# Optimization experiments

Hardware: AMD Instinct MI355X
Metric: run time of the kernel (lower is better)

The kernel has to match this reference:

```python
import jax, jax.numpy as jnp
import numpy as np

EMBED = 2048
NUM_HEADS = 32
HEAD_DIM = EMBED // NUM_HEADS  # 64 (original head dim; sets the scaling)
RANK_KQ = 1024
RANK_V = 1024
DK = RANK_KQ // NUM_HEADS  # 32 low-rank kq head dim
DV = RANK_V // NUM_HEADS   # 32 low-rank v head dim
B, S = 2, 2048


def setup_inputs() -> dict:
    key = jax.random.key(0)
    ks = jax.random.split(key, 10)
    std = 0.02
    hidden_states = jax.random.normal(ks[0], (B, S, EMBED), dtype=jnp.float32)
    # causal additive mask, shape (B, 1, S, S) as asserted in forward
    neg = jnp.finfo(jnp.float32).min
    causal = jnp.where(jnp.tril(jnp.ones((S, S), dtype=bool)), 0.0, neg)
    attention_mask = jnp.broadcast_to(causal[None, None], (B, 1, S, S)).astype(jnp.float32)
    Wq = jax.random.normal(ks[1], (RANK_KQ, EMBED), dtype=jnp.float32) * std
    bq = jax.random.normal(ks[2], (RANK_KQ,), dtype=jnp.float32) * std
    Wk = jax.random.normal(ks[3], (RANK_KQ, EMBED), dtype=jnp.float32) * std
    bk = jax.random.normal(ks[4], (RANK_KQ,), dtype=jnp.float32) * std
    Wv = jax.random.normal(ks[5], (RANK_V, EMBED), dtype=jnp.float32) * std
    bv = jax.random.normal(ks[6], (RANK_V,), dtype=jnp.float32) * std
    Wo = jax.random.normal(ks[7], (EMBED, RANK_V), dtype=jnp.float32) * std
    bo = jax.random.normal(ks[8], (EMBED,), dtype=jnp.float32) * std
    return {"hidden_states": hidden_states, "attention_mask": attention_mask,
            "Wq": Wq, "bq": bq, "Wk": Wk, "bk": bk, "Wv": Wv, "bv": bv,
            "Wo": Wo, "bo": bo}


def reference(hidden_states, attention_mask, Wq, bq, Wk, bk, Wv, bv, Wo, bo):
    bsz, tgt_len, _ = hidden_states.shape
    scaling = HEAD_DIM ** (-0.5)  # uses ORIGINAL head_dim, not low-rank dim

    def split_heads(x, d):  # (b, s, H*d) -> (b, H, s, d)
        return x.reshape(bsz, -1, NUM_HEADS, d).transpose(0, 2, 1, 3)

    q = split_heads((hidden_states @ Wq.T + bq) * scaling, DK)
    k = split_heads(hidden_states @ Wk.T + bk, DK)
    v = split_heads(hidden_states @ Wv.T + bv, DV)

    # scores: (b, H, tgt, src)
    attn = jnp.einsum('bhqd,bhkd->bhqk', q, k)
    attn = attn + attention_mask  # broadcast over heads
    attn = jnp.maximum(attn, jnp.finfo(attn.dtype).min)
    attn = jax.nn.softmax(attn, axis=-1)

    out = jnp.einsum('bhqk,bhkd->bhqd', attn, v)  # (b, H, tgt, DV)
    out = out.transpose(0, 2, 1, 3).reshape(bsz, tgt_len, RANK_V)
    return out @ Wo.T + bo
```

## Files before the change

kernel.cpp:

```cpp
#include <hip/hip_runtime.h>
#include <stdint.h>

typedef __attribute__((ext_vector_type(8))) short bf16x8;
typedef __attribute__((ext_vector_type(4))) float f32x4;
typedef unsigned short ushort_t;

#define AS1 __attribute__((address_space(1)))
#define AS3 __attribute__((address_space(3)))

static __device__ __forceinline__ ushort_t f2b(float f) {
    union { float f; unsigned u; } x; x.f = f;
    unsigned r = x.u + 0x7fffu + ((x.u >> 16) & 1u);
    return (ushort_t)(r >> 16);
}
static __device__ __forceinline__ f32x4 mfma16(bf16x8 a, bf16x8 b, f32x4 c) {
    return __builtin_amdgcn_mfma_f32_16x16x32_bf16(a, b, c, 0, 0, 0);
}
static __device__ __forceinline__ void gl_lds16(const ushort_t* g, ushort_t* l) {
    __builtin_amdgcn_global_load_lds((const AS1 void*)g, (AS3 void*)l, 16, 0, 0);
}

__global__ __launch_bounds__(256)
void cvt_bf16(const float* __restrict__ s, ushort_t* __restrict__ d, int n8)
{
    int i = blockIdx.x * 256 + threadIdx.x;
    if (i >= n8) return;
    const float* p = s + (size_t)i * 8;
    f32x4 a = *(const f32x4*)p;
    f32x4 b = *(const f32x4*)(p + 4);
    bf16x8 r;
#pragma unroll
    for (int j = 0; j < 4; ++j) { r[j] = (short)f2b(a[j]); r[j+4] = (short)f2b(b[j]); }
    *(bf16x8*)(d + (size_t)i * 8) = r;
}

__global__ __launch_bounds__(256)
void cvt_w3(const float* __restrict__ wq, const float* __restrict__ wk,
            const float* __restrict__ wv, ushort_t* __restrict__ d)
{
    const float* s = (blockIdx.y == 0) ? wq : (blockIdx.y == 1) ? wk : wv;
    ushort_t* dst = d + (size_t)blockIdx.y * 2097152;
    int i = blockIdx.x * 256 + threadIdx.x;
    const float* p = s + (size_t)i * 8;
    f32x4 a = *(const f32x4*)p;
    f32x4 b = *(const f32x4*)(p + 4);
    bf16x8 r;
#pragma unroll
    for (int j = 0; j < 4; ++j) { r[j] = (short)f2b(a[j]); r[j+4] = (short)f2b(b[j]); }
    *(bf16x8*)(dst + (size_t)i * 8) = r;
}

__global__ __launch_bounds__(256, 2)
void gemm_nt(const ushort_t* __restrict__ A, const ushort_t* __restrict__ B,
             const float* __restrict__ b0, const float* __restrict__ b1,
             const float* __restrict__ b2, void* __restrict__ Cv,
             int M, int N, int K, float scale, int epi)
{
    __shared__ __align__(16) ushort_t As[128 * 32];
    __shared__ __align__(16) ushort_t Bs[128 * 32];
    const int tid = threadIdx.x;
    const int wave = tid >> 6, lane = tid & 63;
    const int l16 = lane & 15, quad = lane >> 4;
    const int bm = blockIdx.x * 128, bn = blockIdx.y * 128;
    const int wm = (wave >> 1) * 64, wn = (wave & 1) * 64;

    f32x4 acc[4][4];
#pragma unroll
    for (int i = 0; i < 4; ++i)
#pragma unroll
        for (int j = 0; j < 4; ++j) acc[i][j] = (f32x4){0.f, 0.f, 0.f, 0.f};

    for (int k0 = 0; k0 < K; k0 += 32) {
        __syncthreads();
#pragma unroll
        for (int i = 0; i < 2; ++i) {
            int chunk = i * 256 + tid;
            int row = chunk >> 2, c8 = chunk & 3;
            gl_lds16(A + (size_t)(bm + row) * K + k0 + c8 * 8, As + chunk * 8);
            gl_lds16(B + (size_t)(bn + row) * K + k0 + c8 * 8, Bs + chunk * 8);
        }
        __syncthreads();
        bf16x8 af[4], bfr[4];
#pragma unroll
        for (int i = 0; i < 4; ++i)
            af[i] = *(const bf16x8*)(As + (wm + i * 16 + l16) * 32 + quad * 8);
#pragma unroll
        for (int j = 0; j < 4; ++j)
            bfr[j] = *(const bf16x8*)(Bs + (wn + j * 16 + l16) * 32 + quad * 8);
#pragma unroll
        for (int i = 0; i < 4; ++i)
#pragma unroll
            for (int j = 0; j < 4; ++j)
                acc[i][j] = mfma16(af[i], bfr[j], acc[i][j]);
    }

#pragma unroll
    for (int i = 0; i < 4; ++i) {
#pragma unroll
        for (int j = 0; j < 4; ++j) {
            int col = bn + wn + j * 16 + l16;
            if (epi == 0) {
                float bvs = b0[col];
#pragma unroll
                for (int r = 0; r < 4; ++r) {
                    int row = bm + wm + i * 16 + quad * 4 + r;
                    ((float*)Cv)[(size_t)row * N + col] = (acc[i][j][r] + bvs) * scale;
                }
            } else {
                int mat = col >> 10, nc = col & 1023;
                float sc = (mat == 0) ? 0.125f : 1.0f;
                const float* bp = (mat == 0) ? b0 : (mat == 1) ? b1 : b2;
                float bvs = bp[nc];
                int h = nc >> 5, d = nc & 31;
                ushort_t* dst = (ushort_t*)Cv + (size_t)mat * 4194304;
#pragma unroll
                for (int r = 0; r < 4; ++r) {
                    int row = bm + wm + i * 16 + quad * 4 + r;
                    int b = row >> 11, s = row & 2047;
                    float v = (acc[i][j][r] + bvs) * sc;
                    dst[(((size_t)(b * 32 + h) * 2048 + s) << 5) + d] = f2b(v);
                }
            }
        }
    }
}

__global__ __launch_bounds__(256, 4)
void attn(const ushort_t* __restrict__ Q, const ushort_t* __restrict__ Kg,
          const ushort_t* __restrict__ V, ushort_t* __restrict__ Ctx)
{
    __shared__ __align__(16) ushort_t Ks[64 * 40];
    __shared__ __align__(16) ushort_t Vt[32 * 72];
    __shared__ __align__(16) ushort_t Ps[4][32 * 72];
    const int tid = threadIdx.x, wave = tid >> 6, lane = tid & 63;
    const int l16 = lane & 15, quad = lane >> 4;
    const int bh = blockIdx.x;
    const int qt = blockIdx.y;
    const ushort_t* Qh = Q + (size_t)bh * 2048 * 32;
    const ushort_t* Kh = Kg + (size_t)bh * 2048 * 32;
    const ushort_t* Vh = V + (size_t)bh * 2048 * 32;
    const int q0 = qt * 128 + wave * 32;

    bf16x8 qf0 = *(const bf16x8*)(Qh + (size_t)(q0 + l16) * 32 + quad * 8);
    bf16x8 qf1 = *(const bf16x8*)(Qh + (size_t)(q0 + 16 + l16) * 32 + quad * 8);

    f32x4 o00 = (f32x4){0.f,0.f,0.f,0.f}, o01 = o00, o10 = o00, o11 = o00;
    float rs0[4] = {0.f,0.f,0.f,0.f}, rs1[4] = {0.f,0.f,0.f,0.f};

    const int row = tid >> 2, c8 = tid & 3;
    const int nch = 2 * qt + 2;
    for (int c = 0; c < nch; ++c) {
        const int kv0 = c * 64;
        bf16x8 kv8 = *(const bf16x8*)(Kh + (size_t)(kv0 + row) * 32 + c8 * 8);
        bf16x8 vv  = *(const bf16x8*)(Vh + (size_t)(kv0 + row) * 32 + c8 * 8);
        __syncthreads();
        *(bf16x8*)(Ks + row * 40 + c8 * 8) = kv8;
#pragma unroll
        for (int j = 0; j < 8; ++j)
            Vt[(c8 * 8 + j) * 72 + row] = (ushort_t)vv[j];
        __syncthreads();

        if (kv0 <= q0 + 31) {
            f32x4 st0[4], st1[4];
#pragma unroll
            for (int t = 0; t < 4; ++t) {
                bf16x8 kf = *(const bf16x8*)(Ks + (t * 16 + l16) * 40 + quad * 8);
                st0[t] = mfma16(qf0, kf, (f32x4){0.f,0.f,0.f,0.f});
                st1[t] = mfma16(qf1, kf, (f32x4){0.f,0.f,0.f,0.f});
            }
#pragma unroll
            for (int t = 0; t < 4; ++t) {
                const int kk = kv0 + t * 16 + l16;
#pragma unroll
                for (int r = 0; r < 4; ++r) {
                    const int qr = q0 + quad * 4 + r;
                    float p0 = (kk <= qr) ? __expf(st0[t][r]) : 0.f;
                    rs0[r] += p0;
                    Ps[wave][(quad * 4 + r) * 72 + t * 16 + l16] = f2b(p0);
                    float p1 = (kk <= qr + 16) ? __expf(st1[t][r]) : 0.f;
                    rs1[r] += p1;
                    Ps[wave][(16 + quad * 4 + r) * 72 + t * 16 + l16] = f2b(p1);
                }
            }
            asm volatile("s_waitcnt lgkmcnt(0)" ::: "memory");
#pragma unroll
            for (int ks = 0; ks < 2; ++ks) {
                bf16x8 v0 = *(const bf16x8*)(Vt + (l16) * 72 + ks * 32 + quad * 8);
                bf16x8 v1 = *(const bf16x8*)(Vt + (16 + l16) * 72 + ks * 32 + quad * 8);
                bf16x8 p0 = *(const bf16x8*)(&Ps[wave][l16 * 72 + ks * 32 + quad * 8]);
                bf16x8 p1 = *(const bf16x8*)(&Ps[wave][(16 + l16) * 72 + ks * 32 + quad * 8]);
                o00 = mfma16(p0, v0, o00);
                o01 = mfma16(p0, v1, o01);
                o10 = mfma16(p1, v0, o10);
                o11 = mfma16(p1, v1, o11);
            }
        }
    }

#pragma unroll
    for (int r = 0; r < 4; ++r) {
#pragma unroll
        for (int off = 1; off < 16; off <<= 1) {
            rs0[r] += __shfl_xor(rs0[r], off);
            rs1[r] += __shfl_xor(rs1[r], off);
        }
    }

    const int b = bh >> 5, h = bh & 31;
#pragma unroll
    for (int r = 0; r < 4; ++r) {
        const int qr = q0 + quad * 4 + r;
        float inv0 = 1.0f / rs0[r];
        float inv1 = 1.0f / rs1[r];
        size_t base0 = ((size_t)b * 2048 + qr) * 1024 + h * 32;
        size_t base1 = ((size_t)b * 2048 + qr + 16) * 1024 + h * 32;
        Ctx[base0 + l16]      = f2b(o00[r] * inv0);
        Ctx[base0 + 16 + l16] = f2b(o01[r] * inv0);
        Ctx[base1 + l16]      = f2b(o10[r] * inv1);
        Ctx[base1 + 16 + l16] = f2b(o11[r] * inv1);
    }
}

extern "C" void kernel_launch(void* const* d_in, const int* in_sizes, int n_in,
                              void* d_out, int out_size, void* d_ws, size_t ws_size,
                              hipStream_t stream)
{
    const float* H  = (const float*)d_in[0];
    const float* Wq = (const float*)d_in[2];
    const float* bq = (const float*)d_in[3];
    const float* Wk = (const float*)d_in[4];
    const float* bk = (const float*)d_in[5];
    const float* Wv = (const float*)d_in[6];
    const float* bv = (const float*)d_in[7];
    const float* Wo = (const float*)d_in[8];
    const float* bo = (const float*)d_in[9];

    ushort_t* Hb   = (ushort_t*)d_ws;
    ushort_t* Wcat = Hb   + (size_t)8388608;
    ushort_t* Qb   = Wcat + (size_t)6291456;
    ushort_t* Kb   = Qb   + (size_t)4194304;
    ushort_t* Vb   = Kb   + (size_t)4194304;
    ushort_t* Ctx  = Vb   + (size_t)4194304;
    ushort_t* Wob  = Hb;

    dim3 blk(256, 1, 1);
    hipLaunchKernelGGL(cvt_bf16, dim3(4096, 1, 1), blk, 0, stream, H, Hb, 1048576);
    hipLaunchKernelGGL(cvt_w3, dim3(1024, 3, 1), blk, 0, stream, Wq, Wk, Wv, Wcat);

    hipLaunchKernelGGL(gemm_nt, dim3(32, 24, 1), blk, 0, stream,
                       Hb, Wcat, bq, bk, bv, (void*)Qb, 4096, 3072, 2048, 1.0f, 2);

    hipLaunchKernelGGL(cvt_bf16, dim3(1024, 1, 1), blk, 0, stream, Wo, Wob, 262144);

    hipLaunchKernelGGL(attn, dim3(64, 16, 1), blk, 0, stream, Qb, Kb, Vb, Ctx);

    hipLaunchKernelGGL(gemm_nt, dim3(32, 16, 1), blk, 0, stream,
                       Ctx, Wob, bo, bo, bo, d_out, 4096, 2048, 1024, 1.0f, 0);
}
```

Baseline: 299.8 us.

## Store V transposed from QKV GEMM and drop LDS staging in attention

The QKV projection epilogue now writes V in a transposed per-head layout (d-major, seq contiguous) using packed 8-byte stores. The attention kernel then loads K and V fragments straight from global memory into registers, which removes the shared-memory K/V staging, the scalar transpose into LDS, and both block-wide barriers per chunk. It also computes S^T so each lane holds one query column, packs P with v_cvt_pk_bf16_f32 into vectorized LDS writes, skips the mask on fully unmasked chunks, and loops each wave only over its own causal range. The cost is redundant global K/V reads per wave, since the four waves no longer share a staged tile, which depends on cache hits.

```diff
diff --git a/kernel.cpp b/kernel.cpp
--- a/kernel.cpp
+++ b/kernel.cpp
@@ -18,6 +18,11 @@
 }
 static __device__ __forceinline__ void gl_lds16(const ushort_t* g, ushort_t* l) {
     __builtin_amdgcn_global_load_lds((const AS1 void*)g, (AS3 void*)l, 16, 0, 0);
+}
+static __device__ __forceinline__ unsigned pk2(float a, float b) {
+    unsigned r;
+    asm("v_cvt_pk_bf16_f32 %0, %1, %2" : "=v"(r) : "v"(a), "v"(b));
+    return r;
 }
 
 __global__ __launch_bounds__(256)
@@ -108,17 +113,28 @@
                 }
             } else {
                 int mat = col >> 10, nc = col & 1023;
-                float sc = (mat == 0) ? 0.125f : 1.0f;
                 const float* bp = (mat == 0) ? b0 : (mat == 1) ? b1 : b2;
                 float bvs = bp[nc];
                 int h = nc >> 5, d = nc & 31;
-                ushort_t* dst = (ushort_t*)Cv + (size_t)mat * 4194304;
-#pragma unroll
-                for (int r = 0; r < 4; ++r) {
-                    int row = bm + wm + i * 16 + quad * 4 + r;
-                    int b = row >> 11, s = row & 2047;
-                    float v = (acc[i][j][r] + bvs) * sc;
-                    dst[(((size_t)(b * 32 + h) * 2048 + s) << 5) + d] = f2b(v);
+                if (mat == 2) {
+                    int row0 = bm + wm + i * 16 + quad * 4;
+                    int b = row0 >> 11, s = row0 & 2047;
+                    ushort_t* dst = (ushort_t*)Cv + (size_t)2 * 4194304
+                                  + ((size_t)(b * 32 + h) * 32 + d) * 2048 + s;
+                    uint2 w;
+                    w.x = ((unsigned)f2b(acc[i][j][1] + bvs) << 16) | f2b(acc[i][j][0] + bvs);
+                    w.y = ((unsigned)f2b(acc[i][j][3] + bvs) << 16) | f2b(acc[i][j][2] + bvs);
+                    *(uint2*)dst = w;
+                } else {
+                    float sc = (mat == 0) ? 0.125f : 1.0f;
+                    ushort_t* dst = (ushort_t*)Cv + (size_t)mat * 4194304;
+#pragma unroll
+                    for (int r = 0; r < 4; ++r) {
+                        int row = bm + wm + i * 16 + quad * 4 + r;
+                        int b = row >> 11, s = row & 2047;
+                        float v = (acc[i][j][r] + bvs) * sc;
+                        dst[(((size_t)(b * 32 + h) * 2048 + s) << 5) + d] = f2b(v);
+                    }
                 }
             }
         }
@@ -127,91 +143,89 @@
 
 __global__ __launch_bounds__(256, 4)
 void attn(const ushort_t* __restrict__ Q, const ushort_t* __restrict__ Kg,
-          const ushort_t* __restrict__ V, ushort_t* __restrict__ Ctx)
-{
-    __shared__ __align__(16) ushort_t Ks[64 * 40];
-    __shared__ __align__(16) ushort_t Vt[32 * 72];
+          const ushort_t* __restrict__ VT, ushort_t* __restrict__ Ctx)
+{
     __shared__ __align__(16) ushort_t Ps[4][32 * 72];
     const int tid = threadIdx.x, wave = tid >> 6, lane = tid & 63;
-    const int l16 = lane & 15, quad = lane >> 4;
+    const int l16 = lane & 15, quad = lane >> 4, quad4 = quad * 4;
     const int bh = blockIdx.x;
     const int qt = blockIdx.y;
-    const ushort_t* Qh = Q + (size_t)bh * 2048 * 32;
+    const ushort_t* Qh = Q  + (size_t)bh * 2048 * 32;
     const ushort_t* Kh = Kg + (size_t)bh * 2048 * 32;
-    const ushort_t* Vh = V + (size_t)bh * 2048 * 32;
+    const ushort_t* Vh = VT + (size_t)bh * 32 * 2048;
     const int q0 = qt * 128 + wave * 32;
 
     bf16x8 qf0 = *(const bf16x8*)(Qh + (size_t)(q0 + l16) * 32 + quad * 8);
     bf16x8 qf1 = *(const bf16x8*)(Qh + (size_t)(q0 + 16 + l16) * 32 + quad * 8);
 
     f32x4 o00 = (f32x4){0.f,0.f,0.f,0.f}, o01 = o00, o10 = o00, o11 = o00;
-    float rs0[4] = {0.f,0.f,0.f,0.f}, rs1[4] = {0.f,0.f,0.f,0.f};
-
-    const int row = tid >> 2, c8 = tid & 3;
-    const int nch = 2 * qt + 2;
-    for (int c = 0; c < nch; ++c) {
+    float rs0 = 0.f, rs1 = 0.f;
+    ushort_t* P0 = &Ps[wave][0];
+
+    const int nchw = ((q0 + 31) >> 6) + 1;
+    for (int c = 0; c < nchw; ++c) {
         const int kv0 = c * 64;
-        bf16x8 kv8 = *(const bf16x8*)(Kh + (size_t)(kv0 + row) * 32 + c8 * 8);
-        bf16x8 vv  = *(const bf16x8*)(Vh + (size_t)(kv0 + row) * 32 + c8 * 8);
-        __syncthreads();
-        *(bf16x8*)(Ks + row * 40 + c8 * 8) = kv8;
-#pragma unroll
-        for (int j = 0; j < 8; ++j)
-            Vt[(c8 * 8 + j) * 72 + row] = (ushort_t)vv[j];
-        __syncthreads();
-
-        if (kv0 <= q0 + 31) {
-            f32x4 st0[4], st1[4];
+        bf16x8 kf[4];
+#pragma unroll
+        for (int t = 0; t < 4; ++t)
+            kf[t] = *(const bf16x8*)(Kh + (size_t)(kv0 + t * 16 + l16) * 32 + quad * 8);
+        f32x4 st0[4], st1[4];
+#pragma unroll
+        for (int t = 0; t < 4; ++t) {
+            st0[t] = mfma16(kf[t], qf0, (f32x4){0.f,0.f,0.f,0.f});
+            st1[t] = mfma16(kf[t], qf1, (f32x4){0.f,0.f,0.f,0.f});
+        }
+        bf16x8 vA0 = *(const bf16x8*)(Vh + (size_t)l16 * 2048 + kv0 + quad * 8);
+        bf16x8 vA1 = *(const bf16x8*)(Vh + (size_t)l16 * 2048 + kv0 + 32 + quad * 8);
+        bf16x8 vB0 = *(const bf16x8*)(Vh + (size_t)(16 + l16) * 2048 + kv0 + quad * 8);
+        bf16x8 vB1 = *(const bf16x8*)(Vh + (size_t)(16 + l16) * 2048 + kv0 + 32 + quad * 8);
+
+        const int qk0 = q0 + l16 - kv0;
+        auto softmax_pack = [&](bool masked) {
 #pragma unroll
             for (int t = 0; t < 4; ++t) {
-                bf16x8 kf = *(const bf16x8*)(Ks + (t * 16 + l16) * 40 + quad * 8);
-                st0[t] = mfma16(qf0, kf, (f32x4){0.f,0.f,0.f,0.f});
-                st1[t] = mfma16(qf1, kf, (f32x4){0.f,0.f,0.f,0.f});
+                float p0[4], p1[4];
+#pragma unroll
+                for (int r = 0; r < 4; ++r) {
+                    const int kk = t * 16 + quad4 + r;
+                    float e0 = __expf(st0[t][r]);
+                    float e1 = __expf(st1[t][r]);
+                    p0[r] = (!masked || kk <= qk0)      ? e0 : 0.f;
+                    p1[r] = (!masked || kk <= qk0 + 16) ? e1 : 0.f;
+                    rs0 += p0[r]; rs1 += p1[r];
+                }
+                uint2 w0, w1;
+                w0.x = pk2(p0[0], p0[1]); w0.y = pk2(p0[2], p0[3]);
+                w1.x = pk2(p1[0], p1[1]); w1.y = pk2(p1[2], p1[3]);
+                *(uint2*)(P0 + (size_t)l16 * 72 + t * 16 + quad4) = w0;
+                *(uint2*)(P0 + (size_t)(16 + l16) * 72 + t * 16 + quad4) = w1;
             }
-#pragma unroll
-            for (int t = 0; t < 4; ++t) {
-                const int kk = kv0 + t * 16 + l16;
-#pragma unroll
-                for (int r = 0; r < 4; ++r) {
-                    const int qr = q0 + quad * 4 + r;
-                    float p0 = (kk <= qr) ? __expf(st0[t][r]) : 0.f;
-                    rs0[r] += p0;
-                    Ps[wave][(quad * 4 + r) * 72 + t * 16 + l16] = f2b(p0);
-                    float p1 = (kk <= qr + 16) ? __expf(st1[t][r]) : 0.f;
-                    rs1[r] += p1;
-                    Ps[wave][(16 + quad * 4 + r) * 72 + t * 16 + l16] = f2b(p1);
-                }
-            }
-            asm volatile("s_waitcnt lgkmcnt(0)" ::: "memory");
-#pragma unroll
-            for (int ks = 0; ks < 2; ++ks) {
-                bf16x8 v0 = *(const bf16x8*)(Vt + (l16) * 72 + ks * 32 + quad * 8);
-                bf16x8 v1 = *(const bf16x8*)(Vt + (16 + l16) * 72 + ks * 32 + quad * 8);
-                bf16x8 p0 = *(const bf16x8*)(&Ps[wave][l16 * 72 + ks * 32 + quad * 8]);
-                bf16x8 p1 = *(const bf16x8*)(&Ps[wave][(16 + l16) * 72 + ks * 32 + quad * 8]);
-                o00 = mfma16(p0, v0, o00);
-                o01 = mfma16(p0, v1, o01);
-                o10 = mfma16(p1, v0, o10);
-                o11 = mfma16(p1, v1, o11);
-            }
-        }
-    }
-
+        };
+        if (kv0 + 63 <= q0) softmax_pack(false); else softmax_pack(true);
+
+        asm volatile("s_waitcnt lgkmcnt(0)" ::: "memory");
+#pragma unroll
+        for (int ks = 0; ks < 2; ++ks) {
+            bf16x8 pa0 = *(const bf16x8*)(P0 + (size_t)l16 * 72 + ks * 32 + quad * 8);
+            bf16x8 pa1 = *(const bf16x8*)(P0 + (size_t)(16 + l16) * 72 + ks * 32 + quad * 8);
+            bf16x8 va = ks ? vA1 : vA0;
+            bf16x8 vb = ks ? vB1 : vB0;
+            o00 = mfma16(pa0, va, o00);
+            o01 = mfma16(pa0, vb, o01);
+            o10 = mfma16(pa1, va, o10);
+            o11 = mfma16(pa1, vb, o11);
+        }
+    }
+
+    rs0 += __shfl_xor(rs0, 16); rs0 += __shfl_xor(rs0, 32);
+    rs1 += __shfl_xor(rs1, 16); rs1 += __shfl_xor(rs1, 32);
+
+    const int b = bh >> 5, h = bh & 31;
 #pragma unroll
     for (int r = 0; r < 4; ++r) {
-#pragma unroll
-        for (int off = 1; off < 16; off <<= 1) {
-            rs0[r] += __shfl_xor(rs0[r], off);
-            rs1[r] += __shfl_xor(rs1[r], off);
-        }
-    }
-
-    const int b = bh >> 5, h = bh & 31;
-#pragma unroll
-    for (int r = 0; r < 4; ++r) {
-        const int qr = q0 + quad * 4 + r;
-        float inv0 = 1.0f / rs0[r];
-        float inv1 = 1.0f / rs1[r];
+        const int qr = q0 + quad4 + r;
+        float inv0 = 1.0f / __shfl(rs0, quad4 + r);
+        float inv1 = 1.0f / __shfl(rs1, quad4 + r);
         size_t base0 = ((size_t)b * 2048 + qr) * 1024 + h * 32;
         size_t base1 = ((size_t)b * 2048 + qr + 16) * 1024 + h * 32;
         Ctx[base0 + l16]      = f2b(o00[r] * inv0);
@@ -239,8 +253,8 @@
     ushort_t* Wcat = Hb   + (size_t)8388608;
     ushort_t* Qb   = Wcat + (size_t)6291456;
     ushort_t* Kb   = Qb   + (size_t)4194304;
-    ushort_t* Vb   = Kb   + (size_t)4194304;
-    ushort_t* Ctx  = Vb   + (size_t)4194304;
+    ushort_t* Vtb  = Kb   + (size_t)4194304;
+    ushort_t* Ctx  = Vtb  + (size_t)4194304;
     ushort_t* Wob  = Hb;
 
     dim3 blk(256, 1, 1);
@@ -252,7 +266,7 @@
 
     hipLaunchKernelGGL(cvt_bf16, dim3(1024, 1, 1), blk, 0, stream, Wo, Wob, 262144);
 
-    hipLaunchKernelGGL(attn, dim3(64, 16, 1), blk, 0, stream, Qb, Kb, Vb, Ctx);
+    hipLaunchKernelGGL(attn, dim3(64, 16, 1), blk, 0, stream, Qb, Kb, Vtb, Ctx);
 
     hipLaunchKernelGGL(gemm_nt, dim3(32, 16, 1), blk, 0, stream,
                        Ctx, Wob, bo, bo, bo, d_out, 4096, 2048, 1024, 1.0f, 0);
```

Result: faster. 292.0 us (-2.6%).
